# Performance work log

Measured on AMD Instinct MI355X. Metric: run time of the kernel, lower is better.

The kernel has to match this reference:

```python
import jax, jax.numpy as jnp
import numpy as np

N_USERS = 200000
N_MOVIES = 80000
N = N_USERS + N_MOVIES
H = 64
F_MOVIE = 20
E = 1250000
EL = 500000


def setup_inputs() -> dict:
    key = jax.random.key(0)
    ks = jax.random.split(key, 13)
    s = 0.05
    inp = {
        "movie_x": jax.random.normal(ks[0], (N_MOVIES, F_MOVIE), jnp.float32),
        "user_emb": jax.random.normal(ks[1], (N_USERS, H), jnp.float32) * s,
        "movie_emb": jax.random.normal(ks[2], (N_MOVIES, H), jnp.float32) * s,
        "lin_W": jax.random.normal(ks[3], (H, F_MOVIE), jnp.float32) * s,
        "lin_b": jax.random.normal(ks[4], (H,), jnp.float32) * s,
        "W1l": jax.random.normal(ks[5], (H, H), jnp.float32) * s,
        "b1": jax.random.normal(ks[6], (H,), jnp.float32) * s,
        "W1r": jax.random.normal(ks[7], (H, H), jnp.float32) * s,
        "W2l": jax.random.normal(ks[8], (H, H), jnp.float32) * s,
        "b2": jax.random.normal(ks[9], (H,), jnp.float32) * s,
        "W2r": jax.random.normal(ks[10], (H, H), jnp.float32) * s,
        "edge_index": jax.random.randint(ks[11], (2, E), 0, N, jnp.int64),
        "edge_label_index": jnp.stack([
            jax.random.randint(jax.random.fold_in(ks[12], 0), (EL,), 0, N_USERS, jnp.int64),
            jax.random.randint(jax.random.fold_in(ks[12], 1), (EL,), 0, N_MOVIES, jnp.int64),
        ]),
    }
    return inp


def _sage(x, src, dst, Wl, bl, Wr):
    # PyG SAGEConv, mean aggregation: lin_l(mean_{j->i} x_j) + lin_r(x_i)
    msg = x[src]  # [E, H] gather
    agg = jax.ops.segment_sum(msg, dst, num_segments=N)  # [N, H] scatter-add
    deg = jax.ops.segment_sum(jnp.ones((src.shape[0],), x.dtype), dst, num_segments=N)
    mean = agg / jnp.maximum(deg, 1.0)[:, None]
    return mean @ Wl.T + bl + x @ Wr.T


def reference(movie_x, user_emb, movie_emb, lin_W, lin_b,
              W1l, b1, W1r, W2l, b2, W2r, edge_index, edge_label_index):
    # encode: users = embedding lookup (node_id == arange), movies = linear(x) + embedding
    x_user = user_emb
    x_movie = movie_x @ lin_W.T + lin_b + movie_emb
    x = jnp.concatenate([x_user, x_movie], axis=0)  # [N, H]

    src, dst = edge_index[0], edge_index[1]
    x = jax.nn.relu(_sage(x, src, dst, W1l, b1, W1r))
    x = _sage(x, src, dst, W2l, b2, W2r)

    xu = x[:N_USERS]
    xm = x[N_USERS:]
    # dot-product edge scoring over supervision edges
    u = xu[edge_label_index[0]]  # [EL, H]
    m = xm[edge_label_index[1]]  # [EL, H]
    return jnp.sum(u * m, axis=-1)  # [EL]
```

## Files before the change

kernel.cpp:

```cpp
#include <hip/hip_runtime.h>
#include <hip/hip_bf16.h>

#define NU 200000
#define NM 80000
#define NT 280000
#define HD 64
#define FM 20

#define BSHIFT 10
#define NBUCK ((NT + 1023) >> 10)
#define SCHUNK 4096

typedef __attribute__((ext_vector_type(8))) short short8;
typedef __attribute__((ext_vector_type(4))) float floatx4;

__device__ __forceinline__ float bfu2f(unsigned short u) {
    union { unsigned int u; float f; } c; c.u = ((unsigned int)u) << 16; return c.f;
}

__device__ __forceinline__ unsigned short f2bf_raw(float f) {
    union { float f; unsigned int u; } c; c.f = f;
    unsigned int u = c.u + 0x7FFFu + ((c.u >> 16) & 1u);
    return (unsigned short)(u >> 16);
}

__device__ __forceinline__ float ldf(const void* p, long i, int isbf) {
    return isbf ? bfu2f(((const unsigned short*)p)[i]) : ((const float*)p)[i];
}
__device__ __forceinline__ int ldidx(const int* p, long j, int is64) {
    return is64 ? p[2 * j] : p[j];
}

__global__ void probe_kernel(const void* user_emb, const int* ei, int* flags) {
    int t = threadIdx.x;
    int bad = 0;
    for (int i = t; i < 128; i += 64) {
        unsigned short h = ((const unsigned short*)user_emb)[i];
        unsigned int e = (h >> 7) & 0xFF;
        if (e >= 135) bad = 1;
    }
    unsigned long long mf = __ballot(bad != 0);
    int odd_nonzero = 0;
    if (t < 16 && ei[2 * t + 1] != 0) odd_nonzero = 1;
    unsigned long long mi = __ballot(odd_nonzero != 0);
    if (t == 0) {
        flags[0] = (mf == 0) ? 1 : 0;
        flags[1] = (mi == 0) ? 1 : 0;
    }
}

__global__ __launch_bounds__(256) void prep_user(
    const void* __restrict__ user_emb,
    unsigned short* __restrict__ xb,
    const int* __restrict__ flags)
{
    long t = (long)blockIdx.x * 256 + threadIdx.x;
    int isbf = flags[0];
    if (isbf) {
        ((short8*)xb)[t] = ((const short8*)user_emb)[t];
    } else {
        floatx4 a = ((const floatx4*)user_emb)[2 * t];
        floatx4 b = ((const floatx4*)user_emb)[2 * t + 1];
        short8 r;
        r[0] = (short)f2bf_raw(a[0]); r[1] = (short)f2bf_raw(a[1]);
        r[2] = (short)f2bf_raw(a[2]); r[3] = (short)f2bf_raw(a[3]);
        r[4] = (short)f2bf_raw(b[0]); r[5] = (short)f2bf_raw(b[1]);
        r[6] = (short)f2bf_raw(b[2]); r[7] = (short)f2bf_raw(b[3]);
        ((short8*)xb)[t] = r;
    }
}

__global__ __launch_bounds__(256) void prep_movie(
    const void* __restrict__ movie_x,
    const void* __restrict__ movie_emb,
    const void* __restrict__ lin_W,
    const void* __restrict__ lin_b,
    unsigned short* __restrict__ xb,
    const int* __restrict__ flags)
{
    int isbf = flags[0];
    int tid = threadIdx.x;
    int lane = tid & 63;
    int wave = blockIdx.x * 4 + (tid >> 6);
    int m0 = __builtin_amdgcn_readfirstlane(wave << 2);
    if (m0 >= NM) return;

    float wr[FM];
    if (isbf) {
        const unsigned int* p = (const unsigned int*)((const unsigned short*)lin_W + (long)lane * FM);
        #pragma unroll
        for (int i = 0; i < FM / 2; ++i) {
            unsigned int u = p[i];
            wr[2 * i]     = bfu2f((unsigned short)(u & 0xFFFFu));
            wr[2 * i + 1] = bfu2f((unsigned short)(u >> 16));
        }
    } else {
        const floatx4* p = (const floatx4*)((const float*)lin_W + (long)lane * FM);
        #pragma unroll
        for (int i = 0; i < FM / 4; ++i) {
            floatx4 v = p[i];
            wr[4 * i] = v[0]; wr[4 * i + 1] = v[1]; wr[4 * i + 2] = v[2]; wr[4 * i + 3] = v[3];
        }
    }
    float bias = ldf(lin_b, lane, isbf);

    #pragma unroll
    for (int mm = 0; mm < 4; ++mm) {
        int m = m0 + mm;
        float a0 = bias + ldf(movie_emb, (long)m * HD + lane, isbf);
        float a1 = 0.f, a2 = 0.f, a3 = 0.f;
        if (isbf) {
            const unsigned int* mr = (const unsigned int*)((const unsigned short*)movie_x + (long)m * FM);
            #pragma unroll
            for (int kk = 0; kk < FM / 2; ++kk) {
                unsigned int u = mr[kk];
                float x0 = bfu2f((unsigned short)(u & 0xFFFFu));
                float x1 = bfu2f((unsigned short)(u >> 16));
                if (kk & 1) { a2 += x0 * wr[2 * kk]; a3 += x1 * wr[2 * kk + 1]; }
                else        { a0 += x0 * wr[2 * kk]; a1 += x1 * wr[2 * kk + 1]; }
            }
        } else {
            const float* mr = (const float*)movie_x + (long)m * FM;
            #pragma unroll
            for (int k = 0; k < FM; k += 4) {
                a0 += mr[k]     * wr[k];
                a1 += mr[k + 1] * wr[k + 1];
                a2 += mr[k + 2] * wr[k + 2];
                a3 += mr[k + 3] * wr[k + 3];
            }
        }
        xb[(long)(NU + m) * HD + lane] = f2bf_raw((a0 + a1) + (a2 + a3));
    }
}

__global__ __launch_bounds__(512) void blk_hist(
    const int* __restrict__ ei, int E,
    int* __restrict__ blkhist,
    const int* __restrict__ flags)
{
    __shared__ int h[NBUCK];
    int tid = threadIdx.x;
    for (int i = tid; i < NBUCK; i += 512) h[i] = 0;
    __syncthreads();
    int is64 = flags[1];
    long e0 = (long)blockIdx.x * SCHUNK;
    long e1 = e0 + SCHUNK; if (e1 > E) e1 = E;
    for (long j = e0 + tid; j < e1; j += 512) {
        int d = ldidx(ei, (long)E + j, is64);
        atomicAdd(&h[d >> BSHIFT], 1);
    }
    __syncthreads();
    long obase = (long)blockIdx.x * NBUCK;
    for (int i = tid; i < NBUCK; i += 512) blkhist[obase + i] = h[i];
}

__global__ __launch_bounds__(256) void col_scan(
    int* __restrict__ blkhist, int NSB,
    int* __restrict__ bcnt)
{
    __shared__ int larr[2048];
    __shared__ int lsum[256];
    int b = blockIdx.x;
    int t = threadIdx.x;
    for (int i = t; i < NSB; i += 256) larr[i] = blkhist[(long)i * NBUCK + b];
    __syncthreads();
    int C = (NSB + 255) >> 8;
    int beg = t * C;
    int end = beg + C; if (end > NSB) end = NSB; if (beg > NSB) beg = NSB;
    int s = 0;
    for (int i = beg; i < end; ++i) s += larr[i];
    lsum[t] = s;
    __syncthreads();
    for (int off = 1; off < 256; off <<= 1) {
        int v = lsum[t];
        if (t >= off) v += lsum[t - off];
        __syncthreads();
        lsum[t] = v;
        __syncthreads();
    }
    int run = (t == 0) ? 0 : lsum[t - 1];
    for (int i = beg; i < end; ++i) {
        int v = larr[i];
        blkhist[(long)i * NBUCK + b] = run;
        run += v;
    }
    if (t == 0) bcnt[b] = lsum[255];
}

__global__ __launch_bounds__(256) void bucket_scan(
    const int* __restrict__ bcnt, int* __restrict__ bstart, int E)
{
    __shared__ int s[256];
    int t = threadIdx.x;
    int a0 = (2 * t     < NBUCK) ? bcnt[2 * t]     : 0;
    int a1 = (2 * t + 1 < NBUCK) ? bcnt[2 * t + 1] : 0;
    s[t] = a0 + a1;
    __syncthreads();
    for (int off = 1; off < 256; off <<= 1) {
        int v = s[t];
        if (t >= off) v += s[t - off];
        __syncthreads();
        s[t] = v;
        __syncthreads();
    }
    int run = (t == 0) ? 0 : s[t - 1];
    if (2 * t     < NBUCK) bstart[2 * t]     = run;
    if (2 * t + 1 < NBUCK) bstart[2 * t + 1] = run + a0;
    if (t == 0) bstart[NBUCK] = E;
}

__global__ __launch_bounds__(512) void scatter_kernel(
    const int* __restrict__ ei, int E,
    const int* __restrict__ bstart,
    const int* __restrict__ blkhist,
    int* __restrict__ packed,
    const int* __restrict__ flags)
{
    __shared__ int cur[NBUCK];
    int tid = threadIdx.x;
    long obase = (long)blockIdx.x * NBUCK;
    for (int i = tid; i < NBUCK; i += 512) cur[i] = bstart[i] + blkhist[obase + i];
    __syncthreads();
    int is64 = flags[1];
    long e0 = (long)blockIdx.x * SCHUNK;
    long e1 = e0 + SCHUNK; if (e1 > E) e1 = E;
    for (long j = e0 + tid; j < e1; j += 512) {
        int s = ldidx(ei, j, is64);
        int d = ldidx(ei, (long)E + j, is64);
        int b = d >> BSHIFT;
        int pos = atomicAdd(&cur[b], 1);
        packed[pos] = (s << BSHIFT) | (d & ((1 << BSHIFT) - 1));
    }
}

__global__ __launch_bounds__(256) void finefill_kernel(
    const int* __restrict__ bstart,
    const int* __restrict__ packed,
    int* __restrict__ rowptr,
    int* __restrict__ cnt,
    int* __restrict__ srclist)
{
    __shared__ int lcnt[1 << BSHIFT];
    __shared__ int lsum[256];
    int b = blockIdx.x;
    int tid = threadIdx.x;
    int nbase = b << BSHIFT;
    int beg = bstart[b];
    int end = bstart[b + 1];

    for (int i = tid; i < (1 << BSHIFT); i += 256) lcnt[i] = 0;
    __syncthreads();

    for (int j = beg + tid; j < end; j += 256)
        atomicAdd(&lcnt[packed[j] & ((1 << BSHIFT) - 1)], 1);
    __syncthreads();

    int i0 = tid * 4;
    int c0 = lcnt[i0], c1 = lcnt[i0 + 1], c2 = lcnt[i0 + 2], c3 = lcnt[i0 + 3];
    lsum[tid] = c0 + c1 + c2 + c3;
    __syncthreads();
    for (int off = 1; off < 256; off <<= 1) {
        int v = lsum[tid];
        if (tid >= off) v += lsum[tid - off];
        __syncthreads();
        lsum[tid] = v;
        __syncthreads();
    }
    int run = beg + ((tid == 0) ? 0 : lsum[tid - 1]);
    int r0 = run, r1 = r0 + c0, r2 = r1 + c1, r3 = r2 + c2;

    int n0 = nbase + i0;
    if (n0     < NT) { rowptr[n0]     = r0; cnt[n0]     = c0; }
    if (n0 + 1 < NT) { rowptr[n0 + 1] = r1; cnt[n0 + 1] = c1; }
    if (n0 + 2 < NT) { rowptr[n0 + 2] = r2; cnt[n0 + 2] = c2; }
    if (n0 + 3 < NT) { rowptr[n0 + 3] = r3; cnt[n0 + 3] = c3; }

    lcnt[i0] = r0; lcnt[i0 + 1] = r1; lcnt[i0 + 2] = r2; lcnt[i0 + 3] = r3;
    __syncthreads();

    for (int j = beg + tid; j < end; j += 256) {
        int p = packed[j];
        int dl = p & ((1 << BSHIFT) - 1);
        int pos = atomicAdd(&lcnt[dl], 1);
        srclist[pos] = p >> BSHIFT;
    }
}

__global__ __launch_bounds__(256) void gather_mean(
    const unsigned short* __restrict__ x,
    const int* __restrict__ rowptr,
    const int* __restrict__ cnt,
    const int* __restrict__ srclist,
    unsigned short* __restrict__ meanb)
{
    int wid = (blockIdx.x * 256 + threadIdx.x) >> 6;
    int lane = threadIdx.x & 63;
    int g = lane >> 2;
    int sub = lane & 3;
    int n = wid * 16 + g;
    if (n >= NT) return;
    int beg = rowptr[n];
    int deg = cnt[n];

    float acc[16];
    #pragma unroll
    for (int k = 0; k < 16; ++k) acc[k] = 0.f;

    for (int j0 = 0; j0 < deg; j0 += 4) {
        int e = j0 + sub;
        int sv = (e < deg) ? srclist[beg + e] : 0;
        int cq = deg - j0; if (cq > 4) cq = 4;
        short8 r[4][2];
        #pragma unroll
        for (int q = 0; q < 4; ++q) {
            int s = __shfl(sv, (g << 2) | q);
            const short8* p = (const short8*)&x[(long)s * HD + sub * 16];
            r[q][0] = p[0];
            r[q][1] = p[1];
        }
        #pragma unroll
        for (int q = 0; q < 4; ++q) {
            if (q < cq) {
                #pragma unroll
                for (int k = 0; k < 8; ++k) {
                    acc[k]     += bfu2f((unsigned short)r[q][0][k]);
                    acc[k + 8] += bfu2f((unsigned short)r[q][1][k]);
                }
            }
        }
    }

    float rd = 1.0f / fmaxf((float)deg, 1.0f);
    short8 o0, o1;
    #pragma unroll
    for (int k = 0; k < 8; ++k) {
        o0[k] = (short)f2bf_raw(acc[k] * rd);
        o1[k] = (short)f2bf_raw(acc[k + 8] * rd);
    }
    short8* op = (short8*)&meanb[(long)n * HD + sub * 16];
    op[0] = o0;
    op[1] = o1;
}

template <bool RELU>
__global__ __launch_bounds__(256) void combine_kernel(
    const unsigned short* __restrict__ meanb,
    const unsigned short* __restrict__ xin,
    const void* __restrict__ Wl,
    const void* __restrict__ bias,
    const void* __restrict__ Wr,
    unsigned short* __restrict__ out,
    const int* __restrict__ flags)
{
    __shared__ short8 lWl8[HD * HD / 8];
    __shared__ short8 lWr8[HD * HD / 8];
    __shared__ short8 lmean8[HD * HD / 8];
    __shared__ short8 lx8[HD * HD / 8];
    __shared__ float lb[HD];
    unsigned short* lWl  = (unsigned short*)lWl8;
    unsigned short* lWr  = (unsigned short*)lWr8;
    unsigned short* lmean = (unsigned short*)lmean8;
    unsigned short* lx   = (unsigned short*)lx8;

    int tid = threadIdx.x;
    int isbf = flags[0];
    if (isbf) {
        const short8* wl8 = (const short8*)Wl;
        const short8* wr8 = (const short8*)Wr;
        for (int i = tid; i < HD * HD / 8; i += 256) { lWl8[i] = wl8[i]; lWr8[i] = wr8[i]; }
    } else {
        const floatx4* wlf = (const floatx4*)Wl;
        const floatx4* wrf = (const floatx4*)Wr;
        for (int i = tid; i < HD * HD / 8; i += 256) {
            floatx4 a = wlf[2 * i], b = wlf[2 * i + 1];
            short8 r;
            r[0]=(short)f2bf_raw(a[0]); r[1]=(short)f2bf_raw(a[1]); r[2]=(short)f2bf_raw(a[2]); r[3]=(short)f2bf_raw(a[3]);
            r[4]=(short)f2bf_raw(b[0]); r[5]=(short)f2bf_raw(b[1]); r[6]=(short)f2bf_raw(b[2]); r[7]=(short)f2bf_raw(b[3]);
            lWl8[i] = r;
            a = wrf[2 * i]; b = wrf[2 * i + 1];
            r[0]=(short)f2bf_raw(a[0]); r[1]=(short)f2bf_raw(a[1]); r[2]=(short)f2bf_raw(a[2]); r[3]=(short)f2bf_raw(a[3]);
            r[4]=(short)f2bf_raw(b[0]); r[5]=(short)f2bf_raw(b[1]); r[6]=(short)f2bf_raw(b[2]); r[7]=(short)f2bf_raw(b[3]);
            lWr8[i] = r;
        }
    }
    if (tid < HD) lb[tid] = ldf(bias, tid, isbf);

    int tile = blockIdx.x;
    long base = (long)tile * HD * HD;
    const short8* mv = (const short8*)(meanb + base);
    const short8* xv = (const short8*)(xin + base);
    for (int i = tid; i < HD * HD / 8; i += 256) { lmean8[i] = mv[i]; lx8[i] = xv[i]; }
    __syncthreads();

    int w = tid >> 6;
    int lane = tid & 63;
    int mrow = lane & 15;
    int quad = lane >> 4;

    short8 am0 = *(const short8*)&lmean[(w * 16 + mrow) * HD + quad * 8];
    short8 am1 = *(const short8*)&lmean[(w * 16 + mrow) * HD + 32 + quad * 8];
    short8 ax0 = *(const short8*)&lx[(w * 16 + mrow) * HD + quad * 8];
    short8 ax1 = *(const short8*)&lx[(w * 16 + mrow) * HD + 32 + quad * 8];

    floatx4 acc[4];
    #pragma unroll
    for (int ht = 0; ht < 4; ++ht) {
        int h = ht * 16 + mrow;
        short8 bl0 = *(const short8*)&lWl[h * HD + quad * 8];
        short8 bl1 = *(const short8*)&lWl[h * HD + 32 + quad * 8];
        short8 br0 = *(const short8*)&lWr[h * HD + quad * 8];
        short8 br1 = *(const short8*)&lWr[h * HD + 32 + quad * 8];
        floatx4 a = {0.f, 0.f, 0.f, 0.f};
        a = __builtin_amdgcn_mfma_f32_16x16x32_bf16(am0, bl0, a, 0, 0, 0);
        a = __builtin_amdgcn_mfma_f32_16x16x32_bf16(am1, bl1, a, 0, 0, 0);
        a = __builtin_amdgcn_mfma_f32_16x16x32_bf16(ax0, br0, a, 0, 0, 0);
        a = __builtin_amdgcn_mfma_f32_16x16x32_bf16(ax1, br1, a, 0, 0, 0);
        acc[ht] = a;
    }

    #pragma unroll
    for (int ht = 0; ht < 4; ++ht) {
        int h = ht * 16 + mrow;
        float bv = lb[h];
        #pragma unroll
        for (int r = 0; r < 4; ++r) {
            int node = w * 16 + quad * 4 + r;
            float v = acc[ht][r] + bv;
            if (RELU) v = fmaxf(v, 0.0f);
            out[base + node * HD + h] = f2bf_raw(v);
        }
    }
}

__global__ __launch_bounds__(256) void dot_kernel(
    const unsigned short* __restrict__ x2,
    const int* __restrict__ eli,
    void* __restrict__ out,
    int EL,
    const int* __restrict__ flags)
{
    int wid = (blockIdx.x * 256 + threadIdx.x) >> 6;
    long base = (long)wid * 16;
    if (base >= EL) return;
    int lane = threadIdx.x & 63;
    int isbf = flags[0];
    int is64 = flags[1];

    int idxv = 0;
    if (lane < 16)      idxv = ldidx(eli, base + lane, is64);
    else if (lane < 32) idxv = ldidx(eli, (long)EL + base + (lane - 16), is64);

    int e   = lane >> 2;
    int seg = lane & 3;
    int u = __shfl(idxv, e);
    int m = __shfl(idxv, 16 + e);

    const short8* up = (const short8*)(x2 + (long)u * HD + seg * 16);
    const short8* mp = (const short8*)(x2 + (long)(NU + m) * HD + seg * 16);
    short8 a0 = up[0], a1 = up[1];
    short8 b0 = mp[0], b1 = mp[1];

    float p = 0.f;
    #pragma unroll
    for (int j = 0; j < 8; ++j) {
        p += bfu2f((unsigned short)a0[j]) * bfu2f((unsigned short)b0[j]);
        p += bfu2f((unsigned short)a1[j]) * bfu2f((unsigned short)b1[j]);
    }
    p += __shfl_xor(p, 1);
    p += __shfl_xor(p, 2);

    if (seg == 0) {
        long g = base + e;
        if (isbf) ((unsigned short*)out)[g] = f2bf_raw(p);
        else      ((float*)out)[g] = p;
    }
}

extern "C" void kernel_launch(void* const* d_in, const int* in_sizes, int n_in,
                              void* d_out, int out_size, void* d_ws, size_t ws_size,
                              hipStream_t stream)
{
    const void* movie_x   = d_in[0];
    const void* user_emb  = d_in[1];
    const void* movie_emb = d_in[2];
    const void* lin_W     = d_in[3];
    const void* lin_b     = d_in[4];
    const void* W1l       = d_in[5];
    const void* b1        = d_in[6];
    const void* W1r       = d_in[7];
    const void* W2l       = d_in[8];
    const void* b2        = d_in[9];
    const void* W2r       = d_in[10];
    const int* ei  = (const int*)d_in[11];
    const int* eli = (const int*)d_in[12];
    int E  = in_sizes[11] / 2;
    int EL = in_sizes[12] / 2;

    const int NSB = (E + SCHUNK - 1) / SCHUNK;

    char* w = (char*)d_ws;
    unsigned short* xb      = (unsigned short*)w;  w += (size_t)NT * HD * 2;
    unsigned short* meanb   = (unsigned short*)w;  w += (size_t)NT * HD * 2;
    int*            cnt     = (int*)w;             w += (size_t)NT * 4;
    int*            rowptr  = (int*)w;             w += (size_t)NT * 4;
    int*            srclist = (int*)w;             w += (size_t)E * 4;
    int*            packed  = (int*)w;             w += (size_t)E * 4;
    int*            bcnt    = (int*)w;             w += (size_t)(NBUCK + 1) * 4;
    int*            bstart  = (int*)w;             w += (size_t)(NBUCK + 1) * 4;
    int*            blkhist = (int*)w;             w += (size_t)NSB * NBUCK * 4;
    int*            flags   = (int*)w;

    const int user_blocks   = (NU * HD / 8) / 256;
    const int movie_blocks  = NM / 16;
    const int gather_blocks = ((NT / 16) * 64 + 255) / 256;
    const int tile_blocks   = NT / 64;
    const int dot_blocks    = ((EL + 15) / 16 + 3) / 4;

    probe_kernel<<<1, 64, 0, stream>>>(user_emb, ei, flags);

    prep_user<<<user_blocks, 256, 0, stream>>>(user_emb, xb, flags);
    prep_movie<<<movie_blocks, 256, 0, stream>>>(movie_x, movie_emb, lin_W, lin_b, xb, flags);

    blk_hist<<<NSB, 512, 0, stream>>>(ei, E, blkhist, flags);
    col_scan<<<NBUCK, 256, 0, stream>>>(blkhist, NSB, bcnt);
    bucket_scan<<<1, 256, 0, stream>>>(bcnt, bstart, E);
    scatter_kernel<<<NSB, 512, 0, stream>>>(ei, E, bstart, blkhist, packed, flags);
    finefill_kernel<<<NBUCK, 256, 0, stream>>>(bstart, packed, rowptr, cnt, srclist);

    gather_mean<<<gather_blocks, 256, 0, stream>>>(xb, rowptr, cnt, srclist, meanb);
    combine_kernel<true><<<tile_blocks, 256, 0, stream>>>(meanb, xb, W1l, b1, W1r, xb, flags);

    gather_mean<<<gather_blocks, 256, 0, stream>>>(xb, rowptr, cnt, srclist, meanb);
    combine_kernel<false><<<tile_blocks, 256, 0, stream>>>(meanb, xb, W2l, b2, W2r, xb, flags);

    dot_kernel<<<dot_blocks, 256, 0, stream>>>(xb, eli, d_out, EL, flags);
}
```

Measured before the change: 327.2 us.

## Fuse neighbor mean gather into SAGE combine kernel with ping-pong buffers

```diff
diff --git a/kernel.cpp b/kernel.cpp
--- a/kernel.cpp
+++ b/kernel.cpp
@@ -286,84 +286,29 @@
     }
 }
 
-__global__ __launch_bounds__(256) void gather_mean(
-    const unsigned short* __restrict__ x,
+template <bool RELU>
+__global__ __launch_bounds__(256) void sage_layer(
+    const unsigned short* __restrict__ xin,
     const int* __restrict__ rowptr,
     const int* __restrict__ cnt,
     const int* __restrict__ srclist,
-    unsigned short* __restrict__ meanb)
-{
-    int wid = (blockIdx.x * 256 + threadIdx.x) >> 6;
-    int lane = threadIdx.x & 63;
-    int g = lane >> 2;
-    int sub = lane & 3;
-    int n = wid * 16 + g;
-    if (n >= NT) return;
-    int beg = rowptr[n];
-    int deg = cnt[n];
-
-    float acc[16];
-    #pragma unroll
-    for (int k = 0; k < 16; ++k) acc[k] = 0.f;
-
-    for (int j0 = 0; j0 < deg; j0 += 4) {
-        int e = j0 + sub;
-        int sv = (e < deg) ? srclist[beg + e] : 0;
-        int cq = deg - j0; if (cq > 4) cq = 4;
-        short8 r[4][2];
-        #pragma unroll
-        for (int q = 0; q < 4; ++q) {
-            int s = __shfl(sv, (g << 2) | q);
-            const short8* p = (const short8*)&x[(long)s * HD + sub * 16];
-            r[q][0] = p[0];
-            r[q][1] = p[1];
-        }
-        #pragma unroll
-        for (int q = 0; q < 4; ++q) {
-            if (q < cq) {
-                #pragma unroll
-                for (int k = 0; k < 8; ++k) {
-                    acc[k]     += bfu2f((unsigned short)r[q][0][k]);
-                    acc[k + 8] += bfu2f((unsigned short)r[q][1][k]);
-                }
-            }
-        }
-    }
-
-    float rd = 1.0f / fmaxf((float)deg, 1.0f);
-    short8 o0, o1;
-    #pragma unroll
-    for (int k = 0; k < 8; ++k) {
-        o0[k] = (short)f2bf_raw(acc[k] * rd);
-        o1[k] = (short)f2bf_raw(acc[k + 8] * rd);
-    }
-    short8* op = (short8*)&meanb[(long)n * HD + sub * 16];
-    op[0] = o0;
-    op[1] = o1;
-}
-
-template <bool RELU>
-__global__ __launch_bounds__(256) void combine_kernel(
-    const unsigned short* __restrict__ meanb,
-    const unsigned short* __restrict__ xin,
     const void* __restrict__ Wl,
     const void* __restrict__ bias,
     const void* __restrict__ Wr,
-    unsigned short* __restrict__ out,
+    unsigned short* __restrict__ xout,
     const int* __restrict__ flags)
 {
     __shared__ short8 lWl8[HD * HD / 8];
     __shared__ short8 lWr8[HD * HD / 8];
     __shared__ short8 lmean8[HD * HD / 8];
-    __shared__ short8 lx8[HD * HD / 8];
     __shared__ float lb[HD];
     unsigned short* lWl  = (unsigned short*)lWl8;
     unsigned short* lWr  = (unsigned short*)lWr8;
-    unsigned short* lmean = (unsigned short*)lmean8;
-    unsigned short* lx   = (unsigned short*)lx8;
+    unsigned short* lm   = (unsigned short*)lmean8;
 
     int tid = threadIdx.x;
     int isbf = flags[0];
+
     if (isbf) {
         const short8* wl8 = (const short8*)Wl;
         const short8* wr8 = (const short8*)Wr;
@@ -387,22 +332,67 @@
 
     int tile = blockIdx.x;
     long base = (long)tile * HD * HD;
-    const short8* mv = (const short8*)(meanb + base);
-    const short8* xv = (const short8*)(xin + base);
-    for (int i = tid; i < HD * HD / 8; i += 256) { lmean8[i] = mv[i]; lx8[i] = xv[i]; }
-    __syncthreads();
 
     int w = tid >> 6;
     int lane = tid & 63;
     int mrow = lane & 15;
     int quad = lane >> 4;
 
-    short8 am0 = *(const short8*)&lmean[(w * 16 + mrow) * HD + quad * 8];
-    short8 am1 = *(const short8*)&lmean[(w * 16 + mrow) * HD + 32 + quad * 8];
-    short8 ax0 = *(const short8*)&lx[(w * 16 + mrow) * HD + quad * 8];
-    short8 ax1 = *(const short8*)&lx[(w * 16 + mrow) * HD + 32 + quad * 8];
-
-    floatx4 acc[4];
+    const short8* xrow = (const short8*)&xin[base + (long)(w * 16 + mrow) * HD];
+    short8 ax0 = xrow[quad];
+    short8 ax1 = xrow[4 + quad];
+
+    int g = lane >> 2;
+    int sub = lane & 3;
+    int nl = w * 16 + g;
+    int n = tile * 64 + nl;
+    int beg = rowptr[n];
+    int deg = cnt[n];
+
+    float acc[16];
+    #pragma unroll
+    for (int k = 0; k < 16; ++k) acc[k] = 0.f;
+
+    for (int j0 = 0; j0 < deg; j0 += 4) {
+        int e = j0 + sub;
+        int sv = (e < deg) ? srclist[beg + e] : 0;
+        int cq = deg - j0; if (cq > 4) cq = 4;
+        short8 r[4][2];
+        #pragma unroll
+        for (int q = 0; q < 4; ++q) {
+            int s = __shfl(sv, (g << 2) | q);
+            const short8* p = (const short8*)&xin[(long)s * HD + sub * 16];
+            r[q][0] = p[0];
+            r[q][1] = p[1];
+        }
+        #pragma unroll
+        for (int q = 0; q < 4; ++q) {
+            if (q < cq) {
+                #pragma unroll
+                for (int k = 0; k < 8; ++k) {
+                    acc[k]     += bfu2f((unsigned short)r[q][0][k]);
+                    acc[k + 8] += bfu2f((unsigned short)r[q][1][k]);
+                }
+            }
+        }
+    }
+
+    float rd = 1.0f / fmaxf((float)deg, 1.0f);
+    short8 o0, o1;
+    #pragma unroll
+    for (int k = 0; k < 8; ++k) {
+        o0[k] = (short)f2bf_raw(acc[k] * rd);
+        o1[k] = (short)f2bf_raw(acc[k + 8] * rd);
+    }
+    *(short8*)&lm[nl * HD + sub * 16]     = o0;
+    *(short8*)&lm[nl * HD + sub * 16 + 8] = o1;
+
+    __syncthreads();
+
+    short8 am0 = *(const short8*)&lm[(w * 16 + mrow) * HD + quad * 8];
+    short8 am1 = *(const short8*)&lm[(w * 16 + mrow) * HD + 32 + quad * 8];
+
+    floatx4 acc4[4];
     #pragma unroll
     for (int ht = 0; ht < 4; ++ht) {
         int h = ht * 16 + mrow;
@@ -415,7 +405,7 @@
         a = __builtin_amdgcn_mfma_f32_16x16x32_bf16(am1, bl1, a, 0, 0, 0);
         a = __builtin_amdgcn_mfma_f32_16x16x32_bf16(ax0, br0, a, 0, 0, 0);
         a = __builtin_amdgcn_mfma_f32_16x16x32_bf16(ax1, br1, a, 0, 0, 0);
-        acc[ht] = a;
+        acc4[ht] = a;
     }
 
     #pragma unroll
@@ -425,9 +415,9 @@
         #pragma unroll
         for (int r = 0; r < 4; ++r) {
             int node = w * 16 + quad * 4 + r;
-            float v = acc[ht][r] + bv;
+            float v = acc4[ht][r] + bv;
             if (RELU) v = fmaxf(v, 0.0f);
-            out[base + node * HD + h] = f2bf_raw(v);
+            xout[base + node * HD + h] = f2bf_raw(v);
         }
     }
 }
@@ -499,8 +489,8 @@
     const int NSB = (E + SCHUNK - 1) / SCHUNK;
 
     char* w = (char*)d_ws;
-    unsigned short* xb      = (unsigned short*)w;  w += (size_t)NT * HD * 2;
-    unsigned short* meanb   = (unsigned short*)w;  w += (size_t)NT * HD * 2;
+    unsigned short* xb0     = (unsigned short*)w;  w += (size_t)NT * HD * 2;
+    unsigned short* xb1     = (unsigned short*)w;  w += (size_t)NT * HD * 2;
     int*            cnt     = (int*)w;             w += (size_t)NT * 4;
     int*            rowptr  = (int*)w;             w += (size_t)NT * 4;
     int*            srclist = (int*)w;             w += (size_t)E * 4;
@@ -512,14 +502,13 @@
 
     const int user_blocks   = (NU * HD / 8) / 256;
     const int movie_blocks  = NM / 16;
-    const int gather_blocks = ((NT / 16) * 64 + 255) / 256;
     const int tile_blocks   = NT / 64;
     const int dot_blocks    = ((EL + 15) / 16 + 3) / 4;
 
     probe_kernel<<<1, 64, 0, stream>>>(user_emb, ei, flags);
 
-    prep_user<<<user_blocks, 256, 0, stream>>>(user_emb, xb, flags);
-    prep_movie<<<movie_blocks, 256, 0, stream>>>(movie_x, movie_emb, lin_W, lin_b, xb, flags);
+    prep_user<<<user_blocks, 256, 0, stream>>>(user_emb, xb0, flags);
+    prep_movie<<<movie_blocks, 256, 0, stream>>>(movie_x, movie_emb, lin_W, lin_b, xb0, flags);
 
     blk_hist<<<NSB, 512, 0, stream>>>(ei, E, blkhist, flags);
     col_scan<<<NBUCK, 256, 0, stream>>>(blkhist, NSB, bcnt);
@@ -527,11 +516,8 @@
     scatter_kernel<<<NSB, 512, 0, stream>>>(ei, E, bstart, blkhist, packed, flags);
     finefill_kernel<<<NBUCK, 256, 0, stream>>>(bstart, packed, rowptr, cnt, srclist);
 
-    gather_mean<<<gather_blocks, 256, 0, stream>>>(xb, rowptr, cnt, srclist, meanb);
-    combine_kernel<true><<<tile_blocks, 256, 0, stream>>>(meanb, xb, W1l, b1, W1r, xb, flags);
-
-    gather_mean<<<gather_blocks, 256, 0, stream>>>(xb, rowptr, cnt, srclist, meanb);
-    combine_kernel<false><<<tile_blocks, 256, 0, stream>>>(meanb, xb, W2l, b2, W2r, xb, flags);
-
-    dot_kernel<<<dot_blocks, 256, 0, stream>>>(xb, eli, d_out, EL, flags);
-}
+    sage_layer<true><<<tile_blocks, 256, 0, stream>>>(xb0, rowptr, cnt, srclist, W1l, b1, W1r, xb1, flags);
+    sage_layer<false><<<tile_blocks, 256, 0, stream>>>(xb1, rowptr, cnt, srclist, W2l, b2, W2r, xb0, flags);
+
+    dot_kernel<<<dot_blocks, 256, 0, stream>>>(xb0, eli, d_out, EL, flags);
+}
```

Result: faster. 305.7 us (-6.5%).
